# Optimization experiments

Hardware: AMD Instinct MI355X
Metric: run time of the kernel (lower is better)

Reference implementation:

```python
import jax, jax.numpy as jnp
import numpy as np

FEAT_STRIDE = 16
SCALES = (8.0, 16.0, 32.0)
RATIOS = (0.5, 1.0, 2.0)
NEG_TH = 0.3
POS_TH = 0.7
FG_FRACTION = 0.5
RPN_BATCHSIZE = 256
A = 9  # num anchors per location


def generate_anchors(base_size=16, ratios=RATIOS, scales=SCALES):
    """Standard py-faster-rcnn anchor generation (ratio-major, scale-minor)."""
    base = np.array([0.0, 0.0, base_size - 1.0, base_size - 1.0])
    w = base[2] - base[0] + 1.0
    h = base[3] - base[1] + 1.0
    xc = base[0] + 0.5 * (w - 1.0)
    yc = base[1] + 0.5 * (h - 1.0)
    ratios = np.asarray(ratios, dtype=np.float64)
    scales = np.asarray(scales, dtype=np.float64)
    size = w * h
    ws = np.round(np.sqrt(size / ratios))          # [3]
    hs = np.round(ws * ratios)                     # [3]
    ws = (ws[:, None] * scales[None, :]).reshape(-1)  # [9]
    hs = (hs[:, None] * scales[None, :]).reshape(-1)
    anchors = np.stack([xc - 0.5 * (ws - 1.0), yc - 0.5 * (hs - 1.0),
                        xc + 0.5 * (ws - 1.0), yc + 0.5 * (hs - 1.0)], axis=1)
    return anchors.astype(np.float32)  # [9,4]


def _rank_desc(scores, mask):
    """Rank (0 = largest) of each element among masked entries, per row."""
    s = jnp.where(mask, scores, -jnp.inf)
    order = jnp.argsort(-s, axis=1)
    return jnp.argsort(order, axis=1)


def setup_inputs() -> dict:
    key = jax.random.key(0)
    k1, k2, k3, k4, k5, k6 = jax.random.split(key, 6)
    B, K, H, W = 32, 50, 64, 64
    IMG = float(H * FEAT_STRIDE)  # 1024
    rpn_cls_score = jax.random.normal(k1, (B, 2 * A, H, W), dtype=jnp.float32)
    x1 = jax.random.uniform(k2, (B, K)) * (IMG - 220.0)
    y1 = jax.random.uniform(k3, (B, K)) * (IMG - 220.0)
    bw = jax.random.uniform(k4, (B, K)) * 180.0 + 16.0
    bh = jax.random.uniform(k5, (B, K)) * 180.0 + 16.0
    gt_boxes = jnp.stack([x1, y1, x1 + bw, y1 + bh, jnp.ones((B, K))], axis=-1).astype(jnp.float32)
    im_info = jnp.tile(jnp.array([[IMG, IMG, 1.0]], dtype=jnp.float32), (B, 1))
    num_boxes = jax.random.randint(k6, (B,), 1, K + 1).astype(jnp.int32)
    return {"rpn_cls_score": rpn_cls_score, "gt_boxes": gt_boxes,
            "im_info": im_info, "num_boxes": num_boxes}


def reference(rpn_cls_score, gt_boxes, im_info, num_boxes):
    B = gt_boxes.shape[0]
    K = gt_boxes.shape[1]
    H, W = rpn_cls_score.shape[2], rpn_cls_score.shape[3]

    anchors = jnp.asarray(generate_anchors())  # [A,4]
    sx = jnp.arange(W, dtype=jnp.float32) * FEAT_STRIDE
    sy = jnp.arange(H, dtype=jnp.float32) * FEAT_STRIDE
    gx, gy = jnp.meshgrid(sx, sy)  # [H,W]
    shifts = jnp.stack([gx.ravel(), gy.ravel(), gx.ravel(), gy.ravel()], axis=1)  # [HW,4]
    all_anchors = (anchors[None, :, :] + shifts[:, None, :]).reshape(-1, 4)  # [N,4], N=HW*A
    N = all_anchors.shape[0]

    im_h, im_w = im_info[0, 0], im_info[0, 1]
    inside = ((all_anchors[:, 0] >= 0) & (all_anchors[:, 1] >= 0) &
              (all_anchors[:, 2] < im_w) & (all_anchors[:, 3] < im_h))  # [N]

    # pairwise IoU [B,N,K] with +1 pixel convention
    gt4 = gt_boxes[..., :4]
    ax1, ay1, ax2, ay2 = (all_anchors[None, :, None, i] for i in range(4))
    gx1, gy1, gx2, gy2 = (gt4[:, None, :, i] for i in range(4))
    iw = jnp.maximum(jnp.minimum(ax2, gx2) - jnp.maximum(ax1, gx1) + 1.0, 0.0)
    ih = jnp.maximum(jnp.minimum(ay2, gy2) - jnp.maximum(ay1, gy1) + 1.0, 0.0)
    inter = iw * ih
    a_area = ((all_anchors[:, 2] - all_anchors[:, 0] + 1.0) *
              (all_anchors[:, 3] - all_anchors[:, 1] + 1.0))[None, :, None]
    g_area = ((gt4[..., 2] - gt4[..., 0] + 1.0) * (gt4[..., 3] - gt4[..., 1] + 1.0))[:, None, :]
    ov = inter / (a_area + g_area - inter)
    valid = (jnp.arange(K)[None, :] < num_boxes[:, None])  # [B,K]
    ov = jnp.where(valid[:, None, :], ov, -1.0)

    max_ov = ov.max(axis=2)       # [B,N]
    argmax = ov.argmax(axis=2)    # [B,N]
    gt_max = ov.max(axis=1)       # [B,K]
    gt_max = jnp.where(gt_max == 0.0, 1e-5, gt_max)
    best = ((ov == gt_max[:, None, :]) & valid[:, None, :]).any(axis=2)  # [B,N]

    lab = jnp.full((B, N), -1.0, dtype=jnp.float32)
    lab = jnp.where(inside[None, :] & (max_ov < NEG_TH), 0.0, lab)
    lab = jnp.where(inside[None, :] & best, 1.0, lab)
    lab = jnp.where(inside[None, :] & (max_ov >= POS_TH), 1.0, lab)

    # random subsampling of positives / negatives
    skey = jax.random.key(42)
    kf, kb = jax.random.split(skey)
    num_fg = int(FG_FRACTION * RPN_BATCHSIZE)
    fg_mask = lab == 1.0
    rk_fg = _rank_desc(jax.random.uniform(kf, (B, N)), fg_mask)
    lab = jnp.where(fg_mask & (rk_fg >= num_fg), -1.0, lab)
    fg_cnt = (lab == 1.0).sum(axis=1)
    num_bg = RPN_BATCHSIZE - fg_cnt  # [B]
    bg_mask = lab == 0.0
    rk_bg = _rank_desc(jax.random.uniform(kb, (B, N)), bg_mask)
    lab = jnp.where(bg_mask & (rk_bg >= num_bg[:, None]), -1.0, lab)

    assigned = jnp.take_along_axis(gt4, argmax[:, :, None], axis=1)  # [B,N,4]
    ew = all_anchors[:, 2] - all_anchors[:, 0] + 1.0
    eh = all_anchors[:, 3] - all_anchors[:, 1] + 1.0
    ecx = all_anchors[:, 0] + 0.5 * ew
    ecy = all_anchors[:, 1] + 0.5 * eh
    gw = assigned[..., 2] - assigned[..., 0] + 1.0
    gh = assigned[..., 3] - assigned[..., 1] + 1.0
    gcx = assigned[..., 0] + 0.5 * gw
    gcy = assigned[..., 1] + 0.5 * gh
    tgt = jnp.stack([(gcx - ecx[None]) / ew[None], (gcy - ecy[None]) / eh[None],
                     jnp.log(gw / ew[None]), jnp.log(gh / eh[None])], axis=-1)  # [B,N,4]
    tgt = jnp.where(inside[None, :, None], tgt, 0.0)

    in_w = jnp.where((lab == 1.0)[:, :, None], 1.0, 0.0) * jnp.ones((4,), jnp.float32)
    num_examples = (lab >= 0.0).sum(axis=1).astype(jnp.float32)  # [B]
    out_w = jnp.where((lab >= 0.0)[:, :, None], (1.0 / num_examples)[:, None, None], 0.0) \
            * jnp.ones((4,), jnp.float32)

    labels_out = lab.reshape(B, H, W, A).transpose(0, 3, 1, 2).reshape(B, 1, A * H, W)
    tgt_out = tgt.reshape(B, H, W, A * 4).transpose(0, 3, 1, 2)
    in_w_out = in_w.reshape(B, H, W, A * 4).transpose(0, 3, 1, 2)
    out_w_out = out_w.reshape(B, H, W, A * 4).transpose(0, 3, 1, 2)
    return (labels_out, tgt_out, in_w_out, out_w_out)
```

## Files before the change

kernel.cpp:

```cpp
#include <hip/hip_runtime.h>
#include <stdint.h>

#pragma clang fp contract(off)

#define NBATCH 32
#define NK 50
#define NH 64
#define NW 64
#define NA 9
#define NN (NH * NW * NA)
#define BN (NBATCH * NN)
#define HWSZ (NH * NW)
#define BLK_PER_B (NN / 256)

constexpr size_t OFF_AMAX  = 0;
constexpr size_t OFF_PK    = OFF_AMAX + (size_t)BN * 4;
constexpr size_t OFF_GTMAX = OFF_PK + (size_t)BN * 4;
constexpr size_t OFF_NUMEX = OFF_GTMAX + (size_t)NBATCH * NK * 4;
constexpr size_t OFF_THR   = OFF_NUMEX + (size_t)NBATCH * 4;

constexpr size_t OUT_LAB  = 0;
constexpr size_t OUT_TGT  = (size_t)NBATCH * NA * HWSZ;
constexpr size_t OUT_INW  = OUT_TGT + (size_t)NBATCH * NA * 4 * HWSZ;
constexpr size_t OUT_OUTW = OUT_INW + (size_t)NBATCH * NA * 4 * HWSZ;

__constant__ float c_anch[NA][4] = {
    {-84.f, -40.f, 99.f, 55.f},    {-176.f, -88.f, 191.f, 103.f},
    {-360.f, -184.f, 375.f, 199.f}, {-56.f, -56.f, 71.f, 71.f},
    {-120.f, -120.f, 135.f, 135.f}, {-248.f, -248.f, 263.f, 263.f},
    {-36.f, -80.f, 51.f, 95.f},    {-80.f, -168.f, 95.f, 183.f},
    {-168.f, -344.f, 183.f, 359.f}};

struct TF2 { uint32_t a, b; };

__host__ __device__ constexpr uint32_t rotl32(uint32_t x, int d) {
  return (x << d) | (x >> (32 - d));
}

__host__ __device__ constexpr TF2 threefry2x32(uint32_t k0, uint32_t k1,
                                               uint32_t x0, uint32_t x1) {
  uint32_t ks2 = k0 ^ k1 ^ 0x1BD11BDAu;
  x0 += k0; x1 += k1;
  x0 += x1; x1 = rotl32(x1, 13); x1 ^= x0;
  x0 += x1; x1 = rotl32(x1, 15); x1 ^= x0;
  x0 += x1; x1 = rotl32(x1, 26); x1 ^= x0;
  x0 += x1; x1 = rotl32(x1, 6);  x1 ^= x0;
  x0 += k1; x1 += ks2 + 1u;
  x0 += x1; x1 = rotl32(x1, 17); x1 ^= x0;
  x0 += x1; x1 = rotl32(x1, 29); x1 ^= x0;
  x0 += x1; x1 = rotl32(x1, 16); x1 ^= x0;
  x0 += x1; x1 = rotl32(x1, 24); x1 ^= x0;
  x0 += ks2; x1 += k0 + 2u;
  x0 += x1; x1 = rotl32(x1, 13); x1 ^= x0;
  x0 += x1; x1 = rotl32(x1, 15); x1 ^= x0;
  x0 += x1; x1 = rotl32(x1, 26); x1 ^= x0;
  x0 += x1; x1 = rotl32(x1, 6);  x1 ^= x0;
  x0 += k0; x1 += k1 + 3u;
  x0 += x1; x1 = rotl32(x1, 17); x1 ^= x0;
  x0 += x1; x1 = rotl32(x1, 29); x1 ^= x0;
  x0 += x1; x1 = rotl32(x1, 16); x1 ^= x0;
  x0 += x1; x1 = rotl32(x1, 24); x1 ^= x0;
  x0 += k1; x1 += ks2 + 4u;
  x0 += x1; x1 = rotl32(x1, 13); x1 ^= x0;
  x0 += x1; x1 = rotl32(x1, 15); x1 ^= x0;
  x0 += x1; x1 = rotl32(x1, 26); x1 ^= x0;
  x0 += x1; x1 = rotl32(x1, 6);  x1 ^= x0;
  x0 += ks2; x1 += k0 + 5u;
  return TF2{x0, x1};
}

constexpr TF2 KEY_FG = threefry2x32(0u, 42u, 0u, 0u);
constexpr TF2 KEY_BG = threefry2x32(0u, 42u, 0u, 1u);

__device__ inline uint32_t rand23(uint32_t k0, uint32_t k1, uint32_t idx) {
  TF2 r = threefry2x32(k0, k1, 0u, idx);
  return (r.a ^ r.b) >> 9;
}

__device__ inline void anchor_of(int n, float& x1, float& y1, float& x2, float& y2) {
  int a = n % NA;
  int s = n / NA;
  int xx = s % NW;
  int yy = s / NW;
  float sx = (float)(xx * 16);
  float sy = (float)(yy * 16);
  x1 = c_anch[a][0] + sx; y1 = c_anch[a][1] + sy;
  x2 = c_anch[a][2] + sx; y2 = c_anch[a][3] + sy;
}

__device__ inline float iou1(float ax1, float ay1, float ax2, float ay2,
                             float gx1, float gy1, float gx2, float gy2) {
  float iw = fminf(ax2, gx2) - fmaxf(ax1, gx1) + 1.0f;
  iw = fmaxf(iw, 0.0f);
  float ih = fminf(ay2, gy2) - fmaxf(ay1, gy1) + 1.0f;
  ih = fmaxf(ih, 0.0f);
  float inter = iw * ih;
  float aa = (ax2 - ax1 + 1.0f) * (ay2 - ay1 + 1.0f);
  float ga = (gx2 - gx1 + 1.0f) * (gy2 - gy1 + 1.0f);
  return inter / (aa + ga - inter);
}

__global__ __launch_bounds__(256) void k_gtmax(const float* __restrict__ gt,
                                               const int* __restrict__ nbox,
                                               float* __restrict__ gtmax) {
  int b = blockIdx.x / NK;
  int k = blockIdx.x % NK;
  if (k >= nbox[b]) {
    if (threadIdx.x == 0) gtmax[blockIdx.x] = -1.0f;
    return;
  }
  const float* g = gt + ((size_t)b * NK + k) * 5;
  float gx1 = g[0], gy1 = g[1], gx2 = g[2], gy2 = g[3];
  float m = 0.0f;
#pragma unroll
  for (int a = 0; a < NA; ++a) {
    float bx1 = c_anch[a][0], by1 = c_anch[a][1];
    float bx2 = c_anch[a][2], by2 = c_anch[a][3];
    int ix_lo = max(0, (int)floorf((gx1 - 1.0f - bx2) * 0.0625f) - 1);
    int ix_hi = min(NW - 1, (int)ceilf((gx2 + 1.0f - bx1) * 0.0625f) + 1);
    int iy_lo = max(0, (int)floorf((gy1 - 1.0f - by2) * 0.0625f) - 1);
    int iy_hi = min(NH - 1, (int)ceilf((gy2 + 1.0f - by1) * 0.0625f) + 1);
    if (ix_lo > ix_hi || iy_lo > iy_hi) continue;
    int nx = ix_hi - ix_lo + 1;
    int ny = iy_hi - iy_lo + 1;
    int lg = 32 - __clz(nx - 1);
    int tot = ny << lg;
    unsigned mask = (1u << lg) - 1u;
    for (int c = threadIdx.x; c < tot; c += 256) {
      int ixo = c & mask;
      if (ixo >= nx) continue;
      int ix = ix_lo + ixo;
      int iy = iy_lo + (c >> lg);
      float sx = (float)(ix * 16), sy = (float)(iy * 16);
      m = fmaxf(m, iou1(bx1 + sx, by1 + sy, bx2 + sx, by2 + sy, gx1, gy1, gx2, gy2));
    }
  }
  for (int o = 1; o < 64; o <<= 1) m = fmaxf(m, __shfl_xor(m, o));
  __shared__ float ws4[4];
  if ((threadIdx.x & 63) == 0) ws4[threadIdx.x >> 6] = m;
  __syncthreads();
  if (threadIdx.x == 0) {
    m = fmaxf(fmaxf(ws4[0], ws4[1]), fmaxf(ws4[2], ws4[3]));
    if (m == 0.0f) m = 1e-5f;
    gtmax[blockIdx.x] = m;
  }
}

__global__ __launch_bounds__(256) void k_label(const float* __restrict__ gt,
                                               const int* __restrict__ nbox,
                                               const float* __restrict__ gtmax,
                                               const float* __restrict__ iminfo,
                                               unsigned* __restrict__ pkarr,
                                               int* __restrict__ amax) {
  int b = blockIdx.x / BLK_PER_B;
  int n = (blockIdx.x % BLK_PER_B) * 256 + threadIdx.x;
  __shared__ float sg[NK * 5];
  __shared__ float sgm[NK];
  __shared__ float sga[NK];
  if (threadIdx.x < NK * 5) sg[threadIdx.x] = gt[(size_t)b * NK * 5 + threadIdx.x];
  if (threadIdx.x < NK) sgm[threadIdx.x] = gtmax[b * NK + threadIdx.x];
  __syncthreads();
  if (threadIdx.x < NK) {
    float* gg = sg + threadIdx.x * 5;
    sga[threadIdx.x] = (gg[2] - gg[0] + 1.0f) * (gg[3] - gg[1] + 1.0f);
  }
  __syncthreads();

  float ax1, ay1, ax2, ay2;
  anchor_of(n, ax1, ay1, ax2, ay2);
  float aa = (ax2 - ax1 + 1.0f) * (ay2 - ay1 + 1.0f);
  int m = nbox[b];
  float best = -2.0f;
  int bi = 0;
  bool isbest = false;
  for (int k = 0; k < m; ++k) {
    float iw = fminf(ax2, sg[k * 5 + 2]) - fmaxf(ax1, sg[k * 5]) + 1.0f;
    iw = fmaxf(iw, 0.0f);
    float ih = fminf(ay2, sg[k * 5 + 3]) - fmaxf(ay1, sg[k * 5 + 1]) + 1.0f;
    ih = fmaxf(ih, 0.0f);
    float inter = iw * ih;
    float ov = inter / (aa + sga[k] - inter);
    if (ov > best) { best = ov; bi = k; }
    if (ov == sgm[k]) isbest = true;
  }
  float imh = iminfo[0], imw = iminfo[1];
  bool inside = (ax1 >= 0.0f) && (ay1 >= 0.0f) && (ax2 < imw) && (ay2 < imh);
  int lab = -1;
  if (inside) {
    if (best < 0.3f) lab = 0;
    if (isbest) lab = 1;
    if (best >= 0.7f) lab = 1;
  }
  int t = b * NN + n;
  uint32_t kk0 = (lab == 1) ? KEY_FG.a : KEY_BG.a;
  uint32_t kk1 = (lab == 1) ? KEY_FG.b : KEY_BG.b;
  uint32_t v = rand23(kk0, kk1, (uint32_t)t);
  pkarr[t] = (v << 2) | (uint32_t)(lab + 1);
  amax[t] = bi;
}

__global__ __launch_bounds__(1024) void k_select(const unsigned* __restrict__ pkarr,
                                                 float* __restrict__ numex,
                                                 uint4* __restrict__ thr) {
  int b = blockIdx.x;
  int base_lab = b * NN;
  int tid = threadIdx.x;

  __shared__ unsigned hF[4096];
  __shared__ unsigned hB[4096];
  __shared__ unsigned listV[2][1024];
  __shared__ unsigned listI[2][1024];
  __shared__ unsigned waveTot[4];
  __shared__ int sFG, sBG, sCross, sBs[2], sR1[2];
  __shared__ unsigned sCnt[2];
  __shared__ unsigned sV[2], sI[2];
  for (int i = tid; i < 4096; i += 1024) { hF[i] = 0; hB[i] = 0; }
  if (tid == 0) { sFG = 0; sBG = 0; sCnt[0] = 0; sCnt[1] = 0; }
  __syncthreads();

  const uint4* pk4 = (const uint4*)(pkarr + base_lab);

  int cfg = 0, cbg = 0;
  for (int i = tid; i < NN / 4; i += 1024) {
    uint4 P4 = pk4[i];
    unsigned pks[4] = {P4.x, P4.y, P4.z, P4.w};
#pragma unroll
    for (int j = 0; j < 4; ++j) {
      unsigned code = pks[j] & 3u;
      cfg += (code == 2u);
      cbg += (code == 1u);
      if (code == 2u) atomicAdd(&hF[pks[j] >> 13], 1u);
      else if (code == 1u) atomicAdd(&hB[pks[j] >> 13], 1u);
    }
  }
  for (int o = 1; o < 64; o <<= 1) { cfg += __shfl_xor(cfg, o); cbg += __shfl_xor(cbg, o); }
  if ((tid & 63) == 0) { atomicAdd(&sFG, cfg); atomicAdd(&sBG, cbg); }
  __syncthreads();

  int fg = sFG, bg = sBG;
  int fgk = min(fg, 128);
  int Cf = 128;
  int Cb = 256 - fgk;
  if (tid == 0) numex[b] = (float)(fgk + min(bg, Cb));
  bool actF = fg > Cf;
  bool actB = bg > Cb;
  if (!actF && !actB) {
    if (tid == 0) *(&thr[b]) = make_uint4(0u, 0x7FFFFFFFu, 0u, 0x7FFFFFFFu);
    return;
  }

  for (int cls = 0; cls < 2; ++cls) {
    bool act = (cls == 0) ? actF : actB;
    if (!act) continue;
    const unsigned* h = (cls == 0) ? hF : hB;
    unsigned C = (unsigned)((cls == 0) ? Cf : Cb);
    if (tid == 0) sCross = -1;
    __syncthreads();
    unsigned myChunk = 0, suf = 0;
    if (tid < 256) {
      for (int j = 0; j < 16; ++j) myChunk += h[tid * 16 + j];
      unsigned ss = myChunk;
      int lane = tid & 63;
#pragma unroll
      for (int o = 1; o < 64; o <<= 1) {
        unsigned t2 = __shfl_down(ss, o);
        if (lane + o < 64) ss += t2;
      }
      suf = ss;
      if (lane == 0) waveTot[tid >> 6] = ss;
    }
    __syncthreads();
    if (tid < 256) {
      int w = tid >> 6;
      for (int w2 = w + 1; w2 < 4; ++w2) suf += waveTot[w2];
      if (suf >= C) atomicMax(&sCross, tid);
    }
    __syncthreads();
    if (tid == sCross) {
      unsigned cum = suf - myChunk;
      int i = tid * 16 + 15;
      for (;; --i) {
        unsigned c = h[i];
        if (cum + c >= C) break;
        cum += c;
      }
      sBs[cls] = i; sR1[cls] = (int)(C - cum);
    }
    __syncthreads();
  }

  int BsF = actF ? sBs[0] : -1;
  int BsB = actB ? sBs[1] : -1;
  for (int i = tid; i < NN / 4; i += 1024) {
    uint4 P4 = pk4[i];
    unsigned pks[4] = {P4.x, P4.y, P4.z, P4.w};
#pragma unroll
    for (int j = 0; j < 4; ++j) {
      unsigned code = pks[j] & 3u;
      int bk = (int)(pks[j] >> 13);
      int cls = -1;
      if (code == 2u && bk == BsF) cls = 0;
      else if (code == 1u && bk == BsB) cls = 1;
      if (cls >= 0) {
        unsigned p = atomicAdd(&sCnt[cls], 1u);
        if (p < 1024u) { listV[cls][p] = pks[j] >> 2; listI[cls][p] = (unsigned)(4 * i + j); }
      }
    }
  }
  __syncthreads();

  for (int cls = 0; cls < 2; ++cls) {
    bool act = (cls == 0) ? actF : actB;
    if (!act) continue;
    unsigned L = min(sCnt[cls], 1024u);
    unsigned target = (unsigned)(sR1[cls] - 1);
    for (unsigned i = tid; i < L; i += 1024) {
      unsigned vi = listV[cls][i], xi = listI[cls][i];
      unsigned rank = 0;
      for (unsigned j = 0; j < L; ++j) {
        unsigned vj = listV[cls][j], xj = listI[cls][j];
        rank += (vj > vi) || (vj == vi && xj < xi);
      }
      if (rank == target) { sV[cls] = vi; sI[cls] = xi; }
    }
  }
  __syncthreads();
  if (tid == 0) {
    uint4 t;
    t.x = actF ? sV[0] : 0u;  t.y = actF ? sI[0] : 0x7FFFFFFFu;
    t.z = actB ? sV[1] : 0u;  t.w = actB ? sI[1] : 0x7FFFFFFFu;
    thr[b] = t;
  }
}

__global__ __launch_bounds__(256) void k_out(const float* __restrict__ gt,
                                             const unsigned* __restrict__ pkarr,
                                             const int* __restrict__ amax,
                                             const float* __restrict__ iminfo,
                                             const float* __restrict__ numex,
                                             const uint4* __restrict__ thr,
                                             float* __restrict__ out) {
  int q = blockIdx.x * 256 + threadIdx.x;
  if (q >= (int)(OUT_TGT / 4)) return;
  int xx4 = q & 15;
  int yy = (q >> 4) & 63;
  int ba = q >> 10;
  int a = ba % NA;
  int b = ba / NA;
  int xx0 = xx4 * 4;
  int yx0 = yy * NW + xx0;

  float imh = iminfo[0], imw = iminfo[1];
  float inv_ne = 1.0f / numex[b];
  uint4 th = thr[b];

  float labf[4], iwv[4], owv[4], tg[4][4];
#pragma unroll
  for (int u = 0; u < 4; ++u) {
    int xx = xx0 + u;
    int n = (yy * NW + xx) * NA + a;
    int bn = b * NN + n;
    unsigned pk = pkarr[bn];
    int lab = (int)(pk & 3u) - 1;
    if (lab >= 0) {
      unsigned v = pk >> 2;
      unsigned vs = (lab == 1) ? th.x : th.z;
      unsigned is = (lab == 1) ? th.y : th.w;
      bool keep = (v > vs) || (v == vs && (unsigned)n <= is);
      if (!keep) lab = -1;
    }
    labf[u] = (float)lab;
    float ax1, ay1, ax2, ay2;
    anchor_of(n, ax1, ay1, ax2, ay2);
    bool inside = (ax1 >= 0.0f) && (ay1 >= 0.0f) && (ax2 < imw) && (ay2 < imh);
    float t0 = 0.f, t1 = 0.f, t2 = 0.f, t3 = 0.f;
    if (inside) {
      const float* g = gt + ((size_t)b * NK + amax[bn]) * 5;
      float ew = ax2 - ax1 + 1.0f, eh = ay2 - ay1 + 1.0f;
      float ecx = ax1 + 0.5f * ew, ecy = ay1 + 0.5f * eh;
      float gw = g[2] - g[0] + 1.0f, gh = g[3] - g[1] + 1.0f;
      float gcx = g[0] + 0.5f * gw, gcy = g[1] + 0.5f * gh;
      t0 = (gcx - ecx) / ew;
      t1 = (gcy - ecy) / eh;
      t2 = logf(gw / ew);
      t3 = logf(gh / eh);
    }
    tg[0][u] = t0; tg[1][u] = t1; tg[2][u] = t2; tg[3][u] = t3;
    iwv[u] = (lab == 1) ? 1.0f : 0.0f;
    owv[u] = (lab >= 0) ? inv_ne : 0.0f;
  }

  *(float4*)(out + OUT_LAB + (size_t)ba * HWSZ + yx0) =
      make_float4(labf[0], labf[1], labf[2], labf[3]);
  size_t tb = OUT_TGT + ((size_t)b * NA * 4 + a * 4) * HWSZ + yx0;
#pragma unroll
  for (int d = 0; d < 4; ++d)
    *(float4*)(out + tb + (size_t)d * HWSZ) =
        make_float4(tg[d][0], tg[d][1], tg[d][2], tg[d][3]);
  size_t ib = OUT_INW + ((size_t)b * NA * 4 + a * 4) * HWSZ + yx0;
  float4 iw4 = make_float4(iwv[0], iwv[1], iwv[2], iwv[3]);
#pragma unroll
  for (int d = 0; d < 4; ++d) *(float4*)(out + ib + (size_t)d * HWSZ) = iw4;
  size_t ob = OUT_OUTW + ((size_t)b * NA * 4 + a * 4) * HWSZ + yx0;
  float4 ow4 = make_float4(owv[0], owv[1], owv[2], owv[3]);
#pragma unroll
  for (int d = 0; d < 4; ++d) *(float4*)(out + ob + (size_t)d * HWSZ) = ow4;
}

extern "C" void kernel_launch(void* const* d_in, const int* in_sizes, int n_in,
                              void* d_out, int out_size, void* d_ws, size_t ws_size,
                              hipStream_t stream) {
  (void)in_sizes; (void)n_in; (void)out_size; (void)ws_size;
  const float* gt     = (const float*)d_in[1];
  const float* iminfo = (const float*)d_in[2];
  const int*   nbox   = (const int*)d_in[3];
  float* out = (float*)d_out;
  char* ws = (char*)d_ws;

  int*      amax  = (int*)(ws + OFF_AMAX);
  unsigned* pkarr = (unsigned*)(ws + OFF_PK);
  float*    gtmax = (float*)(ws + OFF_GTMAX);
  float*    numex = (float*)(ws + OFF_NUMEX);
  uint4*    thr   = (uint4*)(ws + OFF_THR);

  k_gtmax<<<NBATCH * NK, 256, 0, stream>>>(gt, nbox, gtmax);
  k_label<<<BN / 256, 256, 0, stream>>>(gt, nbox, gtmax, iminfo, pkarr, amax);
  k_select<<<NBATCH, 1024, 0, stream>>>(pkarr, numex, thr);
  k_out<<<(int)(OUT_TGT / 4 / 256), 256, 0, stream>>>(gt, pkarr, amax, iminfo, numex, thr, out);
}
```

Baseline: 162.8 us.

## Store labels anchor-major and cull GT boxes per block in k_label

Each k_label block now handles one anchor type over 256 cells (four rows) and keeps only the GT boxes whose y-range can overlap those rows, compacted into shared memory with a ballot. This cuts the per-anchor IoU loop. The packed label and argmax arrays are stored in (a, cell) order, so k_out reads them with coalesced vector loads and k_select maps indices back to the original anchor order for its tie-breaks. In exchange the intermediate layout changes, and the best-IoU start value moves from -2 to 0, so correctness depends on the culling being exact.

```diff
diff --git a/kernel.cpp b/kernel.cpp
--- a/kernel.cpp
+++ b/kernel.cpp
@@ -11,7 +11,6 @@
 #define NN (NH * NW * NA)
 #define BN (NBATCH * NN)
 #define HWSZ (NH * NW)
-#define BLK_PER_B (NN / 256)
 
 constexpr size_t OFF_AMAX  = 0;
 constexpr size_t OFF_PK    = OFF_AMAX + (size_t)BN * 4;
@@ -77,17 +76,6 @@
   return (r.a ^ r.b) >> 9;
 }
 
-__device__ inline void anchor_of(int n, float& x1, float& y1, float& x2, float& y2) {
-  int a = n % NA;
-  int s = n / NA;
-  int xx = s % NW;
-  int yy = s / NW;
-  float sx = (float)(xx * 16);
-  float sy = (float)(yy * 16);
-  x1 = c_anch[a][0] + sx; y1 = c_anch[a][1] + sy;
-  x2 = c_anch[a][2] + sx; y2 = c_anch[a][3] + sy;
-}
-
 __device__ inline float iou1(float ax1, float ay1, float ax2, float ay2,
                              float gx1, float gy1, float gx2, float gy2) {
   float iw = fminf(ax2, gx2) - fmaxf(ax1, gx1) + 1.0f;
@@ -150,38 +138,63 @@
                                                const int* __restrict__ nbox,
                                                const float* __restrict__ gtmax,
                                                const float* __restrict__ iminfo,
-                                               unsigned* __restrict__ pkarr,
-                                               int* __restrict__ amax) {
-  int b = blockIdx.x / BLK_PER_B;
-  int n = (blockIdx.x % BLK_PER_B) * 256 + threadIdx.x;
-  __shared__ float sg[NK * 5];
-  __shared__ float sgm[NK];
-  __shared__ float sga[NK];
-  if (threadIdx.x < NK * 5) sg[threadIdx.x] = gt[(size_t)b * NK * 5 + threadIdx.x];
-  if (threadIdx.x < NK) sgm[threadIdx.x] = gtmax[b * NK + threadIdx.x];
-  __syncthreads();
-  if (threadIdx.x < NK) {
-    float* gg = sg + threadIdx.x * 5;
-    sga[threadIdx.x] = (gg[2] - gg[0] + 1.0f) * (gg[3] - gg[1] + 1.0f);
-  }
-  __syncthreads();
-
-  float ax1, ay1, ax2, ay2;
-  anchor_of(n, ax1, ay1, ax2, ay2);
-  float aa = (ax2 - ax1 + 1.0f) * (ay2 - ay1 + 1.0f);
-  int m = nbox[b];
-  float best = -2.0f;
+                                               unsigned* __restrict__ pk2,
+                                               int* __restrict__ amax2) {
+  int bid = blockIdx.x;
+  int b = bid / (NA * 16);
+  int rem = bid - b * (NA * 16);
+  int a = rem >> 4;
+  int cell0 = (rem & 15) << 8;
+  float bx1 = c_anch[a][0], by1 = c_anch[a][1];
+  float bx2 = c_anch[a][2], by2 = c_anch[a][3];
+  int tid = threadIdx.x;
+
+  __shared__ float cx1[NK], cy1[NK], cx2[NK], cy2[NK], cga[NK], cgm[NK];
+  __shared__ int ckk[NK];
+  __shared__ int cN;
+  if (tid < 64) {
+    int m = nbox[b];
+    bool keep = false;
+    float gx1 = 0, gy1 = 0, gx2 = 0, gy2 = 0, gm = 0;
+    if (tid < m) {
+      const float* g = gt + ((size_t)b * NK + tid) * 5;
+      gx1 = g[0]; gy1 = g[1]; gx2 = g[2]; gy2 = g[3];
+      gm = gtmax[b * NK + tid];
+      float sy0 = (float)((cell0 >> 6) << 4);
+      float lo = fmaxf(by1 + sy0, gy1);
+      float hi = fminf(by2 + sy0 + 48.0f, gy2);
+      keep = (hi - lo + 2.0f) > 0.0f;
+    }
+    unsigned long long mk = __ballot(keep);
+    if (keep) {
+      int pos = (int)__popcll(mk & ((1ull << tid) - 1ull));
+      cx1[pos] = gx1; cy1[pos] = gy1; cx2[pos] = gx2; cy2[pos] = gy2;
+      cga[pos] = (gx2 - gx1 + 1.0f) * (gy2 - gy1 + 1.0f);
+      cgm[pos] = gm; ckk[pos] = tid;
+    }
+    if (tid == 0) cN = (int)__popcll(mk);
+  }
+  __syncthreads();
+
+  int cell = cell0 + tid;
+  float sx = (float)((cell & 63) << 4);
+  float sy = (float)((cell >> 6) << 4);
+  float ax1 = bx1 + sx, ay1 = by1 + sy;
+  float ax2 = bx2 + sx, ay2 = by2 + sy;
+  float aa = (bx2 - bx1 + 1.0f) * (by2 - by1 + 1.0f);
+  float best = 0.0f;
   int bi = 0;
   bool isbest = false;
-  for (int k = 0; k < m; ++k) {
-    float iw = fminf(ax2, sg[k * 5 + 2]) - fmaxf(ax1, sg[k * 5]) + 1.0f;
+  int M = cN;
+  for (int j = 0; j < M; ++j) {
+    float iw = fminf(ax2, cx2[j]) - fmaxf(ax1, cx1[j]) + 1.0f;
     iw = fmaxf(iw, 0.0f);
-    float ih = fminf(ay2, sg[k * 5 + 3]) - fmaxf(ay1, sg[k * 5 + 1]) + 1.0f;
+    float ih = fminf(ay2, cy2[j]) - fmaxf(ay1, cy1[j]) + 1.0f;
     ih = fmaxf(ih, 0.0f);
     float inter = iw * ih;
-    float ov = inter / (aa + sga[k] - inter);
-    if (ov > best) { best = ov; bi = k; }
-    if (ov == sgm[k]) isbest = true;
+    float ov = inter / (aa + cga[j] - inter);
+    if (ov > best) { best = ov; bi = ckk[j]; }
+    isbest |= (ov == cgm[j]);
   }
   float imh = iminfo[0], imw = iminfo[1];
   bool inside = (ax1 >= 0.0f) && (ay1 >= 0.0f) && (ax2 < imw) && (ay2 < imh);
@@ -191,15 +204,16 @@
     if (isbest) lab = 1;
     if (best >= 0.7f) lab = 1;
   }
-  int t = b * NN + n;
+  int n = cell * NA + a;
   uint32_t kk0 = (lab == 1) ? KEY_FG.a : KEY_BG.a;
   uint32_t kk1 = (lab == 1) ? KEY_FG.b : KEY_BG.b;
-  uint32_t v = rand23(kk0, kk1, (uint32_t)t);
-  pkarr[t] = (v << 2) | (uint32_t)(lab + 1);
-  amax[t] = bi;
-}
-
-__global__ __launch_bounds__(1024) void k_select(const unsigned* __restrict__ pkarr,
+  uint32_t v = rand23(kk0, kk1, (uint32_t)(b * NN + n));
+  int tp = b * NN + a * HWSZ + cell;
+  pk2[tp] = (v << 2) | (uint32_t)(lab + 1);
+  amax2[tp] = bi;
+}
+
+__global__ __launch_bounds__(1024) void k_select(const unsigned* __restrict__ pk2,
                                                  float* __restrict__ numex,
                                                  uint4* __restrict__ thr) {
   int b = blockIdx.x;
@@ -218,7 +232,7 @@
   if (tid == 0) { sFG = 0; sBG = 0; sCnt[0] = 0; sCnt[1] = 0; }
   __syncthreads();
 
-  const uint4* pk4 = (const uint4*)(pkarr + base_lab);
+  const uint4* pk4 = (const uint4*)(pk2 + base_lab);
 
   int cfg = 0, cbg = 0;
   for (int i = tid; i < NN / 4; i += 1024) {
@@ -245,7 +259,7 @@
   bool actF = fg > Cf;
   bool actB = bg > Cb;
   if (!actF && !actB) {
-    if (tid == 0) *(&thr[b]) = make_uint4(0u, 0x7FFFFFFFu, 0u, 0x7FFFFFFFu);
+    if (tid == 0) thr[b] = make_uint4(0u, 0x7FFFFFFFu, 0u, 0x7FFFFFFFu);
     return;
   }
 
@@ -302,8 +316,10 @@
       if (code == 2u && bk == BsF) cls = 0;
       else if (code == 1u && bk == BsB) cls = 1;
       if (cls >= 0) {
+        int f = 4 * i + j;
+        unsigned n = (unsigned)((f & 4095) * NA + (f >> 12));
         unsigned p = atomicAdd(&sCnt[cls], 1u);
-        if (p < 1024u) { listV[cls][p] = pks[j] >> 2; listI[cls][p] = (unsigned)(4 * i + j); }
+        if (p < 1024u) { listV[cls][p] = pks[j] >> 2; listI[cls][p] = n; }
       }
     }
   }
@@ -334,8 +350,8 @@
 }
 
 __global__ __launch_bounds__(256) void k_out(const float* __restrict__ gt,
-                                             const unsigned* __restrict__ pkarr,
-                                             const int* __restrict__ amax,
+                                             const unsigned* __restrict__ pk2,
+                                             const int* __restrict__ amax2,
                                              const float* __restrict__ iminfo,
                                              const float* __restrict__ numex,
                                              const uint4* __restrict__ thr,
@@ -354,13 +370,22 @@
   float inv_ne = 1.0f / numex[b];
   uint4 th = thr[b];
 
+  int t4 = ba * HWSZ + yx0;
+  uint4 pkq = *(const uint4*)(pk2 + t4);
+  int4 amq = *(const int4*)(amax2 + t4);
+  unsigned pkv[4] = {pkq.x, pkq.y, pkq.z, pkq.w};
+  int amv[4] = {amq.x, amq.y, amq.z, amq.w};
+
+  float bx1 = c_anch[a][0], by1 = c_anch[a][1];
+  float bx2 = c_anch[a][2], by2 = c_anch[a][3];
+  float sy = (float)(yy * 16);
+
   float labf[4], iwv[4], owv[4], tg[4][4];
 #pragma unroll
   for (int u = 0; u < 4; ++u) {
     int xx = xx0 + u;
     int n = (yy * NW + xx) * NA + a;
-    int bn = b * NN + n;
-    unsigned pk = pkarr[bn];
+    unsigned pk = pkv[u];
     int lab = (int)(pk & 3u) - 1;
     if (lab >= 0) {
       unsigned v = pk >> 2;
@@ -370,12 +395,12 @@
       if (!keep) lab = -1;
     }
     labf[u] = (float)lab;
-    float ax1, ay1, ax2, ay2;
-    anchor_of(n, ax1, ay1, ax2, ay2);
+    float sx = (float)(xx * 16);
+    float ax1 = bx1 + sx, ay1 = by1 + sy, ax2 = bx2 + sx, ay2 = by2 + sy;
     bool inside = (ax1 >= 0.0f) && (ay1 >= 0.0f) && (ax2 < imw) && (ay2 < imh);
     float t0 = 0.f, t1 = 0.f, t2 = 0.f, t3 = 0.f;
     if (inside) {
-      const float* g = gt + ((size_t)b * NK + amax[bn]) * 5;
+      const float* g = gt + ((size_t)b * NK + amv[u]) * 5;
       float ew = ax2 - ax1 + 1.0f, eh = ay2 - ay1 + 1.0f;
       float ecx = ax1 + 0.5f * ew, ecy = ay1 + 0.5f * eh;
       float gw = g[2] - g[0] + 1.0f, gh = g[3] - g[1] + 1.0f;
@@ -417,14 +442,14 @@
   float* out = (float*)d_out;
   char* ws = (char*)d_ws;
 
-  int*      amax  = (int*)(ws + OFF_AMAX);
-  unsigned* pkarr = (unsigned*)(ws + OFF_PK);
+  int*      amax2 = (int*)(ws + OFF_AMAX);
+  unsigned* pk2   = (unsigned*)(ws + OFF_PK);
   float*    gtmax = (float*)(ws + OFF_GTMAX);
   float*    numex = (float*)(ws + OFF_NUMEX);
   uint4*    thr   = (uint4*)(ws + OFF_THR);
 
   k_gtmax<<<NBATCH * NK, 256, 0, stream>>>(gt, nbox, gtmax);
-  k_label<<<BN / 256, 256, 0, stream>>>(gt, nbox, gtmax, iminfo, pkarr, amax);
-  k_select<<<NBATCH, 1024, 0, stream>>>(pkarr, numex, thr);
-  k_out<<<(int)(OUT_TGT / 4 / 256), 256, 0, stream>>>(gt, pkarr, amax, iminfo, numex, thr, out);
-}
+  k_label<<<NBATCH * NA * 16, 256, 0, stream>>>(gt, nbox, gtmax, iminfo, pk2, amax2);
+  k_select<<<NBATCH, 1024, 0, stream>>>(pk2, numex, thr);
+  k_out<<<(int)(OUT_TGT / 4 / 256), 256, 0, stream>>>(gt, pk2, amax2, iminfo, numex, thr, out);
+}
```

Result: faster. 145.2 us (-10.8%).
